# Kernel optimization log

Measured on AMD Instinct MI355X. Metric: run time of the kernel, lower is better.

Reference implementation:

```python
import jax, jax.numpy as jnp
from jax import lax
import numpy as np

WSTD = 0.1
BSTD = 0.1
DN = ("NHWC", "HWIO", "NHWC")  # matches tf.nn.convolution defaults


def setup_inputs() -> dict:
    key = jax.random.key(0)
    k1, k2, k3, k4, k5 = jax.random.split(key, 5)
    B, H, Wd, Cin, F, KH, KW = 32, 64, 64, 128, 256, 3, 3
    X = jax.random.normal(k1, (B, H, Wd, Cin), dtype=jnp.float32)
    # glorot-ish kernel
    fan = KH * KW * Cin
    W = jax.random.normal(k2, (KH, KW, Cin, F), dtype=jnp.float32) / np.float32(np.sqrt(fan))
    bias = 0.01 * jax.random.normal(k3, (F,), dtype=jnp.float32)
    # per-sample multiplicative errors: abs(1 + N(0, std)) as in A-Connect
    Werr = jnp.abs(1.0 + WSTD * jax.random.normal(k4, (B, KH, KW, Cin, F), dtype=jnp.float32))
    Berr = jnp.abs(1.0 + BSTD * jax.random.normal(k5, (B, F), dtype=jnp.float32))
    return {"X": X, "W": W, "bias": bias, "Werr": Werr, "Berr": Berr}


def reference(X, W, bias, Werr, Berr):
    # memW[b] = W * Werr[b]  -> per-sample perturbed kernels [B,KH,KW,Cin,F]
    memW = W[None] * Werr

    def conv1(x, k):  # x: [H,W,Cin], k: [KH,KW,Cin,F]
        return lax.conv_general_dilated(x[None], k, window_strides=(1, 1),
                                        padding="SAME", dimension_numbers=DN)[0]

    Z = jax.vmap(conv1)(X, memW)                 # [B,H,W,F]
    membias = bias[None] * Berr                  # [B,F]
    Z = Z + membias[:, None, None, :]
    return jax.nn.relu(Z)
```

## Files before the change

kernel.cpp:

```cpp
#include <hip/hip_runtime.h>

#define B_   32
#define H_   64
#define W_   64
#define CIN  128
#define F_   256
#define K_   1152
#define M_   4096

#define HP_   66
#define XPROW (66*128)
#define XPIMG (66*66*128)
#define XP_ELEMS ((size_t)B_ * XPIMG)
#define XP_BYTES (XP_ELEMS * 2)

#define WBT_BYTES ((size_t)B_ * F_ * K_ * 2)
#define FULL_WS   (WBT_BYTES + XP_BYTES + 256)
#define ZPAGE_OFF WBT_BYTES

#define BM_ 256
#define BK_ 64

typedef __attribute__((ext_vector_type(8))) short bf16x8;
typedef __attribute__((ext_vector_type(4))) float f32x4;

__device__ __forceinline__ unsigned pkbf(float a, float b) {
    unsigned ua = __builtin_bit_cast(unsigned, a) + 0x8000u;
    unsigned ub = __builtin_bit_cast(unsigned, b) + 0x8000u;
    return __builtin_amdgcn_perm(ub, ua, 0x07060302u);
}

__device__ __forceinline__ void async16(const void* g, void* l) {
    __builtin_amdgcn_global_load_lds(
        (const __attribute__((address_space(1))) unsigned int*)g,
        (__attribute__((address_space(3))) unsigned int*)l, 16, 0, 0);
}

__global__ void prep_kernel(const float* __restrict__ W,
                            const float* __restrict__ Werr,
                            const float* __restrict__ X,
                            unsigned short* __restrict__ WbT,
                            unsigned short* __restrict__ Xp,
                            unsigned int* __restrict__ zpage) {
    __shared__ float tile[32 * 68];
    int bid = blockIdx.x;
    int t   = threadIdx.x;

    if (bid < 4608) {
        int ft   = bid & 3;
        int rest = bid >> 2;
        int kt   = rest % 36;
        int b    = rest / 36;
        int k0 = kt * 32;
        int f0 = ft * 64;

        if (bid == 0 && t < 64) zpage[t] = 0u;

        #pragma unroll
        for (int i = 0; i < 2; ++i) {
            int c   = i * 256 + t;
            int kl  = c >> 4;
            int fl4 = c & 15;
            size_t src = (size_t)(k0 + kl) * F_ + f0 + fl4 * 4;
            f32x4 w4 = *(const f32x4*)&W[src];
            f32x4 e4 = *(const f32x4*)&Werr[(size_t)b * (K_ * F_) + src];
            f32x4 v  = w4 * e4;
            *(f32x4*)&tile[kl * 68 + fl4 * 4] = v;
        }
        __syncthreads();
        {
            int c  = t;
            int fl = c >> 2;
            int ku = c & 3;
            unsigned pk[4];
            #pragma unroll
            for (int j2 = 0; j2 < 4; ++j2) {
                float x0 = tile[(ku * 8 + j2 * 2 + 0) * 68 + fl];
                float x1 = tile[(ku * 8 + j2 * 2 + 1) * 68 + fl];
                pk[j2] = pkbf(x0, x1);
            }
            size_t dst = ((size_t)(b * F_ + f0 + fl)) * K_ + k0 + ku * 8;
            *(uint4*)&WbT[dst] = make_uint4(pk[0], pk[1], pk[2], pk[3]);
        }
    } else {
        int e = (bid - 4608) * 256 + t;
        int c16  = e & 15;
        int pos  = e >> 4;
        int wp   = pos % 66;
        int rest = pos / 66;
        int hp   = rest % 66;
        int b    = rest / 66;
        uint4 out;
        if (hp >= 1 && hp <= 64 && wp >= 1 && wp <= 64) {
            const float* src = X + (((size_t)b * 64 + (hp - 1)) * 64 + (wp - 1)) * 128
                                 + c16 * 8;
            f32x4 a = *(const f32x4*)src;
            f32x4 c = *(const f32x4*)(src + 4);
            out.x = pkbf(a[0], a[1]);  out.y = pkbf(a[2], a[3]);
            out.z = pkbf(c[0], c[1]);  out.w = pkbf(c[2], c[3]);
        } else {
            out = make_uint4(0u, 0u, 0u, 0u);
        }
        *(uint4*)&Xp[(size_t)e * 8] = out;
    }
}

__global__ void wbt_kernel(const float* __restrict__ W,
                           const float* __restrict__ Werr,
                           unsigned short* __restrict__ WbT,
                           unsigned int* __restrict__ zpage) {
    __shared__ float tile[32 * 68];
    int bid = blockIdx.x;
    int ft   = bid & 3;
    int rest = bid >> 2;
    int kt   = rest % 36;
    int b    = rest / 36;
    int k0 = kt * 32;
    int f0 = ft * 64;
    int t  = threadIdx.x;

    if (bid == 0 && t < 64) zpage[t] = 0u;

    #pragma unroll
    for (int i = 0; i < 2; ++i) {
        int c   = i * 256 + t;
        int kl  = c >> 4;
        int fl4 = c & 15;
        size_t src = (size_t)(k0 + kl) * F_ + f0 + fl4 * 4;
        f32x4 w4 = *(const f32x4*)&W[src];
        f32x4 e4 = *(const f32x4*)&Werr[(size_t)b * (K_ * F_) + src];
        f32x4 v  = w4 * e4;
        *(f32x4*)&tile[kl * 68 + fl4 * 4] = v;
    }
    __syncthreads();
    {
        int c  = t;
        int fl = c >> 2;
        int ku = c & 3;
        unsigned pk[4];
        #pragma unroll
        for (int j2 = 0; j2 < 4; ++j2) {
            float x0 = tile[(ku * 8 + j2 * 2 + 0) * 68 + fl];
            float x1 = tile[(ku * 8 + j2 * 2 + 1) * 68 + fl];
            pk[j2] = pkbf(x0, x1);
        }
        size_t dst = ((size_t)(b * F_ + f0 + fl)) * K_ + k0 + ku * 8;
        *(uint4*)&WbT[dst] = make_uint4(pk[0], pk[1], pk[2], pk[3]);
    }
}

__global__ __launch_bounds__(512, 2)
void gemm256_kernel(const unsigned short* __restrict__ Xp,
                    const unsigned short* __restrict__ WbT,
                    const float* __restrict__ bias,
                    const float* __restrict__ Berr,
                    float* __restrict__ Out) {
    __shared__ unsigned short As[2][BM_ * BK_];
    __shared__ unsigned short Bs[2][BM_ * BK_];

    int bid = blockIdx.x;
    int g   = (bid & 7) * 64 + (bid >> 3);
    int b   = g >> 4;
    int mt  = g & 15;
    int pm0 = mt * 256;

    int t    = threadIdx.x;
    int lane = t & 63;
    int wv   = t >> 6;
    int wm   = wv >> 2;
    int wn   = wv & 3;
    int l16  = lane & 15;
    int quad = lane >> 4;
    int swz  = (l16 & 7) << 4;

    const unsigned short* XpB = Xp + (size_t)b * XPIMG;
    const unsigned short* WbB = WbT + (size_t)b * F_ * K_;

    int tr   = t >> 3;
    int sc   = (t & 7) ^ (tr & 7);
    int aoff = tr * 128 + sc * 8;
    int boff = tr * K_ + sc * 8;
    int mbase = mt * 4;
    int ldof = t * 8;

    f32x4 acc[8][4];
    #pragma unroll
    for (int mi = 0; mi < 8; ++mi)
        #pragma unroll
        for (int ni = 0; ni < 4; ++ni)
            acc[mi][ni] = (f32x4){0.f, 0.f, 0.f, 0.f};

    auto stageA = [&](int bs, int ru, int ko) {
        async16(XpB + (size_t)(mbase + ru) * XPROW + aoff + ko,
                &As[bs][ru * 4096 + ldof]);
    };
    auto stageB = [&](int bs, int ru, int ko) {
        async16(WbB + (size_t)ru * (64 * K_) + boff + ko,
                &Bs[bs][ru * 4096 + ldof]);
    };

    stageB(0, 0, 0); stageB(0, 1, 0); stageB(0, 2, 0); stageB(0, 3, 0);
    stageA(0, 0, 0); stageA(0, 2, 0); stageA(0, 1, 0); stageA(0, 3, 0);
    asm volatile("s_waitcnt vmcnt(2)" ::: "memory");
    __builtin_amdgcn_s_barrier();

    for (int kt = 0; kt < 18; ++kt) {
        const int cur = kt & 1;
        const int nxt = cur ^ 1;
        const unsigned short* Ac = As[cur];
        const unsigned short* Bc = Bs[cur];
        const bool pf = (kt < 17);

        int ktn  = kt + 1;
        int khwN = ktn >> 1;
        int khN  = (khwN * 11) >> 5;
        int kwN  = khwN - khN * 3;
        int koA  = khN * XPROW + kwN * 128 + (ktn & 1) * 64;
        int koB  = ktn * 64;

        bf16x8 af[4], bfr[4];

        #pragma unroll
        for (int ni = 0; ni < 4; ++ni) {
            int row = wn * 64 + ni * 16 + l16;
            bfr[ni] = *(const bf16x8*)((const char*)Bc + ((row * 128 + quad * 16) ^ swz));
        }
        #pragma unroll
        for (int mi = 0; mi < 4; ++mi) {
            int row = wm * 128 + mi * 16 + l16;
            af[mi] = *(const bf16x8*)((const char*)Ac + ((row * 128 + quad * 16) ^ swz));
        }
        if (pf) { stageB(nxt, 0, koB); stageB(nxt, 1, koB); }
        __builtin_amdgcn_s_barrier();
        __builtin_amdgcn_s_setprio(1);
        #pragma unroll
        for (int mi = 0; mi < 4; ++mi)
            #pragma unroll
            for (int ni = 0; ni < 4; ++ni)
                acc[mi][ni] = __builtin_amdgcn_mfma_f32_16x16x32_bf16(
                    af[mi], bfr[ni], acc[mi][ni], 0, 0, 0);
        __builtin_amdgcn_s_setprio(0);
        if (pf) asm volatile("s_waitcnt vmcnt(2)" ::: "memory");
        else    asm volatile("s_waitcnt vmcnt(0)" ::: "memory");
        __builtin_amdgcn_s_barrier();

        #pragma unroll
        for (int mi = 0; mi < 4; ++mi) {
            int row = wm * 128 + 64 + mi * 16 + l16;
            af[mi] = *(const bf16x8*)((const char*)Ac + ((row * 128 + quad * 16) ^ swz));
        }
        if (pf) { stageB(nxt, 2, koB); stageB(nxt, 3, koB); }
        __builtin_amdgcn_s_barrier();
        __builtin_amdgcn_s_setprio(1);
        #pragma unroll
        for (int mi = 0; mi < 4; ++mi)
            #pragma unroll
            for (int ni = 0; ni < 4; ++ni)
                acc[4 + mi][ni] = __builtin_amdgcn_mfma_f32_16x16x32_bf16(
                    af[mi], bfr[ni], acc[4 + mi][ni], 0, 0, 0);
        __builtin_amdgcn_s_setprio(0);
        __builtin_amdgcn_s_barrier();

        #pragma unroll
        for (int ni = 0; ni < 4; ++ni) {
            int row = wn * 64 + ni * 16 + l16;
            bfr[ni] = *(const bf16x8*)((const char*)Bc + ((row * 128 + quad * 16 + 64) ^ swz));
        }
        #pragma unroll
        for (int mi = 0; mi < 4; ++mi) {
            int row = wm * 128 + mi * 16 + l16;
            af[mi] = *(const bf16x8*)((const char*)Ac + ((row * 128 + quad * 16 + 64) ^ swz));
        }
        if (pf) { stageA(nxt, 0, koA); stageA(nxt, 2, koA); }
        __builtin_amdgcn_s_barrier();
        __builtin_amdgcn_s_setprio(1);
        #pragma unroll
        for (int mi = 0; mi < 4; ++mi)
            #pragma unroll
            for (int ni = 0; ni < 4; ++ni)
                acc[mi][ni] = __builtin_amdgcn_mfma_f32_16x16x32_bf16(
                    af[mi], bfr[ni], acc[mi][ni], 0, 0, 0);
        __builtin_amdgcn_s_setprio(0);
        __builtin_amdgcn_s_barrier();

        #pragma unroll
        for (int mi = 0; mi < 4; ++mi) {
            int row = wm * 128 + 64 + mi * 16 + l16;
            af[mi] = *(const bf16x8*)((const char*)Ac + ((row * 128 + quad * 16 + 64) ^ swz));
        }
        if (pf) { stageA(nxt, 1, koA); stageA(nxt, 3, koA); }
        __builtin_amdgcn_s_barrier();
        __builtin_amdgcn_s_setprio(1);
        #pragma unroll
        for (int mi = 0; mi < 4; ++mi)
            #pragma unroll
            for (int ni = 0; ni < 4; ++ni)
                acc[4 + mi][ni] = __builtin_amdgcn_mfma_f32_16x16x32_bf16(
                    af[mi], bfr[ni], acc[4 + mi][ni], 0, 0, 0);
        __builtin_amdgcn_s_setprio(0);
        if (pf) asm volatile("s_waitcnt vmcnt(2)" ::: "memory");
        __builtin_amdgcn_s_barrier();
    }

    float mb[4];
    #pragma unroll
    for (int ni = 0; ni < 4; ++ni) {
        int f = wn * 64 + ni * 16 + l16;
        mb[ni] = bias[f] * Berr[b * F_ + f];
    }
    #pragma unroll
    for (int mi = 0; mi < 8; ++mi) {
        #pragma unroll
        for (int rr = 0; rr < 4; ++rr) {
            int mm = pm0 + wm * 128 + mi * 16 + quad * 4 + rr;
            float* orow = Out + ((size_t)b * M_ + mm) * F_ + wn * 64;
            #pragma unroll
            for (int ni = 0; ni < 4; ++ni) {
                float v = acc[mi][ni][rr] + mb[ni];
                orow[ni * 16 + l16] = fmaxf(v, 0.0f);
            }
        }
    }
}

__global__ __launch_bounds__(256, 2)
void gemm_kernel_f32(const float* __restrict__ X,
                     const unsigned short* __restrict__ WbT,
                     const float* __restrict__ zpage,
                     const float* __restrict__ bias,
                     const float* __restrict__ Berr,
                     float* __restrict__ Out) {
    __shared__ unsigned short As[128 * 32];
    __shared__ unsigned short Bs[128 * 32];

    int bid = blockIdx.x;
    int g   = (bid & 7) | ((bid >> 8) << 3);
    int mt  = (bid >> 3) & 31;
    int b   = g >> 1;
    int nt  = g & 1;
    int pm0 = mt * 128;

    int t    = threadIdx.x;
    int lane = t & 63;
    int wv   = t >> 6;
    int wm   = wv >> 1;
    int wn   = wv & 1;
    int l16  = lane & 15;
    int quad = lane >> 4;

    int ml   = t >> 1;
    int half = t & 1;
    int m    = pm0 + ml;
    int hb   = m >> 6;
    int wwv  = m & 63;
    const float* Abase = X + (((size_t)b * 64 + hb - 1) * 64 + (wwv - 1)) * 128
                           + half * 16;
    unsigned vm = 0;
    #pragma unroll
    for (int khw = 0; khw < 9; ++khw) {
        int kh = (khw * 11) >> 5;
        int kw = khw - kh * 3;
        bool ok = ((unsigned)(hb + kh - 1) < 64u) && ((unsigned)(wwv + kw - 1) < 64u);
        vm |= (unsigned)ok << khw;
    }
    int ldsA = ml * 32 + half * 16;

    const unsigned short* wb = WbT + ((size_t)(b * F_ + nt * 128)) * K_;
    const unsigned short* Bbase[2];
    int ldsB[2];
    #pragma unroll
    for (int cc = 0; cc < 2; ++cc) {
        int c   = t + cc * 256;
        int nl  = c >> 2;
        int off = c & 3;
        Bbase[cc] = wb + (size_t)nl * K_ + off * 8;
        ldsB[cc]  = c * 8;
    }

    f32x4 acc[4][4];
    #pragma unroll
    for (int mi = 0; mi < 4; ++mi)
        #pragma unroll
        for (int ni = 0; ni < 4; ++ni)
            acc[mi][ni] = (f32x4){0.f, 0.f, 0.f, 0.f};

    f32x4 pr0, pr1, pr2, pr3;
    {
        const float* p = (vm & 1) ? Abase : zpage;
        pr0 = *(const f32x4*)(p);
        pr1 = *(const f32x4*)(p + 4);
        pr2 = *(const f32x4*)(p + 8);
        pr3 = *(const f32x4*)(p + 12);
    }

    for (int kt = 0; kt < 36; ++kt) {
        uint4 lo, hi;
        lo.x = pkbf(pr0[0], pr0[1]);  lo.y = pkbf(pr0[2], pr0[3]);
        lo.z = pkbf(pr1[0], pr1[1]);  lo.w = pkbf(pr1[2], pr1[3]);
        hi.x = pkbf(pr2[0], pr2[1]);  hi.y = pkbf(pr2[2], pr2[3]);
        hi.z = pkbf(pr3[0], pr3[1]);  hi.w = pkbf(pr3[2], pr3[3]);

        if (kt) __syncthreads();
        *(uint4*)&As[ldsA]     = lo;
        *(uint4*)&As[ldsA + 8] = hi;
        #pragma unroll
        for (int cc = 0; cc < 2; ++cc)
            async16(Bbase[cc] + kt * 32, &Bs[ldsB[cc]]);
        __syncthreads();

        if (kt < 35) {
            int ktn  = kt + 1;
            int khw  = ktn >> 2;
            int kh   = (khw * 11) >> 5;
            int kw   = khw - kh * 3;
            int koff = kh * 8192 + kw * 128 + ((ktn & 3) << 5);
            const float* p = ((vm >> khw) & 1) ? Abase + koff : zpage;
            pr0 = *(const f32x4*)(p);
            pr1 = *(const f32x4*)(p + 4);
            pr2 = *(const f32x4*)(p + 8);
            pr3 = *(const f32x4*)(p + 12);
        }

        bf16x8 af[4], bf[4];
        #pragma unroll
        for (int i = 0; i < 4; ++i) {
            af[i] = *(const bf16x8*)&As[(wm * 64 + i * 16 + l16) * 32 + quad * 8];
            bf[i] = *(const bf16x8*)&Bs[(wn * 64 + i * 16 + l16) * 32 + quad * 8];
        }
        #pragma unroll
        for (int mi = 0; mi < 4; ++mi)
            #pragma unroll
            for (int ni = 0; ni < 4; ++ni)
                acc[mi][ni] = __builtin_amdgcn_mfma_f32_16x16x32_bf16(
                    af[mi], bf[ni], acc[mi][ni], 0, 0, 0);
    }

    float mb[4];
    #pragma unroll
    for (int ni = 0; ni < 4; ++ni) {
        int f = nt * 128 + wn * 64 + ni * 16 + l16;
        mb[ni] = bias[f] * Berr[b * F_ + f];
    }
    #pragma unroll
    for (int mi = 0; mi < 4; ++mi) {
        #pragma unroll
        for (int rr = 0; rr < 4; ++rr) {
            int mm = pm0 + wm * 64 + mi * 16 + quad * 4 + rr;
            float* orow = Out + ((size_t)b * M_ + mm) * F_ + nt * 128 + wn * 64;
            #pragma unroll
            for (int ni = 0; ni < 4; ++ni) {
                float v = acc[mi][ni][rr] + mb[ni];
                orow[ni * 16 + l16] = fmaxf(v, 0.0f);
            }
        }
    }
}

__global__ __launch_bounds__(256)
void fallback_kernel(const float* __restrict__ X, const float* __restrict__ W,
                     const float* __restrict__ bias, const float* __restrict__ Werr,
                     const float* __restrict__ Berr, float* __restrict__ Out) {
    __shared__ float Xs[3 * 66 * 128];
    int bid = blockIdx.x;
    int b = bid >> 6;
    int h = bid & 63;
    int t = threadIdx.x;
    int f = t;

    for (int e = t; e < 3 * 66 * 128; e += 256) {
        int kh  = e / (66 * 128);
        int rem = e - kh * 66 * 128;
        int w66 = rem >> 7;
        int c   = rem & 127;
        int hh = h + kh - 1, ww = w66 - 1;
        float v = 0.f;
        if (hh >= 0 && hh < 64 && ww >= 0 && ww < 64)
            v = X[(((size_t)b * 64 + hh) * 64 + ww) * 128 + c];
        Xs[e] = v;
    }
    __syncthreads();

    float acc[64];
    #pragma unroll
    for (int w = 0; w < 64; ++w) acc[w] = 0.f;

    for (int kk = 0; kk < 9; ++kk) {
        int kh = (kk * 11) >> 5;
        int kw = kk - kh * 3;
        for (int c = 0; c < 128; ++c) {
            size_t wi = ((size_t)kk * 128 + c) * 256 + f;
            float wvv = W[wi] * Werr[(size_t)b * (K_ * F_) + wi];
            const float* xr = &Xs[(kh * 66 + kw) * 128 + c];
            #pragma unroll
            for (int w = 0; w < 64; ++w)
                acc[w] = fmaf(xr[w * 128], wvv, acc[w]);
        }
    }
    float mb = bias[f] * Berr[b * 256 + f];
    for (int w = 0; w < 64; ++w)
        Out[(((size_t)b * 64 + h) * 64 + w) * 256 + f] = fmaxf(acc[w] + mb, 0.f);
}

extern "C" void kernel_launch(void* const* d_in, const int* in_sizes, int n_in,
                              void* d_out, int out_size, void* d_ws, size_t ws_size,
                              hipStream_t stream) {
    const float* X    = (const float*)d_in[0];
    const float* W    = (const float*)d_in[1];
    const float* bias = (const float*)d_in[2];
    const float* Werr = (const float*)d_in[3];
    const float* Berr = (const float*)d_in[4];
    float* Out = (float*)d_out;

    if (ws_size >= FULL_WS) {
        unsigned short* WbT = (unsigned short*)d_ws;
        unsigned short* Xp  = (unsigned short*)((char*)d_ws + WBT_BYTES);
        unsigned int*   zpg = (unsigned int*)((char*)d_ws + WBT_BYTES + XP_BYTES);
        prep_kernel<<<4608 + 8712, 256, 0, stream>>>(W, Werr, X, WbT, Xp, zpg);
        gemm256_kernel<<<512, 512, 0, stream>>>(Xp, WbT, bias, Berr, Out);
    } else if (ws_size >= WBT_BYTES + 256) {
        unsigned short* WbT  = (unsigned short*)d_ws;
        unsigned int*   zpg  = (unsigned int*)((char*)d_ws + ZPAGE_OFF);
        wbt_kernel<<<B_ * 36 * 4, 256, 0, stream>>>(W, Werr, WbT, zpg);
        gemm_kernel_f32<<<B_ * 32 * 2, 256, 0, stream>>>(X, WbT, (const float*)zpg,
                                                         bias, Berr, Out);
    } else {
        fallback_kernel<<<B_ * 64, 256, 0, stream>>>(X, W, bias, Werr, Berr, Out);
    }
}
```

Baseline: 297.0 us.

## Restructure GEMM k-loop: fewer barriers, batched async staging, separate fragment registers

The inner k-tile loop drops from eight workgroup barriers per iteration to two. Each half of the tile's async global-to-LDS copies for B and A is now issued in one batch instead of being spread across four phases. Distinct register fragments (a0..a3, b0, b1) are kept so LDS reads can be grouped and MFMAs issued back-to-back, and sched_barrier pins the compiler ordering. This cuts barrier stalls at the cost of higher VGPR pressure and less interleaving of copies with compute.

Result: faster. 289.3 us (-2.6%).

```diff
diff --git a/kernel.cpp b/kernel.cpp
--- a/kernel.cpp
+++ b/kernel.cpp
@@ -203,6 +203,7 @@
     stageA(0, 0, 0); stageA(0, 2, 0); stageA(0, 1, 0); stageA(0, 3, 0);
     asm volatile("s_waitcnt vmcnt(2)" ::: "memory");
     __builtin_amdgcn_s_barrier();
+    __builtin_amdgcn_sched_barrier(0);
 
     for (int kt = 0; kt < 18; ++kt) {
         const int cur = kt & 1;
@@ -218,88 +219,90 @@
         int koA  = khN * XPROW + kwN * 128 + (ktn & 1) * 64;
         int koB  = ktn * 64;
 
-        bf16x8 af[4], bfr[4];
-
+        bf16x8 b0[4], a0[4];
         #pragma unroll
         for (int ni = 0; ni < 4; ++ni) {
             int row = wn * 64 + ni * 16 + l16;
-            bfr[ni] = *(const bf16x8*)((const char*)Bc + ((row * 128 + quad * 16) ^ swz));
+            b0[ni] = *(const bf16x8*)((const char*)Bc + ((row * 128 + quad * 16) ^ swz));
         }
         #pragma unroll
         for (int mi = 0; mi < 4; ++mi) {
             int row = wm * 128 + mi * 16 + l16;
-            af[mi] = *(const bf16x8*)((const char*)Ac + ((row * 128 + quad * 16) ^ swz));
-        }
-        if (pf) { stageB(nxt, 0, koB); stageB(nxt, 1, koB); }
-        __builtin_amdgcn_s_barrier();
+            a0[mi] = *(const bf16x8*)((const char*)Ac + ((row * 128 + quad * 16) ^ swz));
+        }
+        if (pf) {
+            stageB(nxt, 0, koB); stageB(nxt, 1, koB);
+            stageB(nxt, 2, koB); stageB(nxt, 3, koB);
+        }
         __builtin_amdgcn_s_setprio(1);
         #pragma unroll
         for (int mi = 0; mi < 4; ++mi)
             #pragma unroll
             for (int ni = 0; ni < 4; ++ni)
                 acc[mi][ni] = __builtin_amdgcn_mfma_f32_16x16x32_bf16(
-                    af[mi], bfr[ni], acc[mi][ni], 0, 0, 0);
+                    a0[mi], b0[ni], acc[mi][ni], 0, 0, 0);
         __builtin_amdgcn_s_setprio(0);
-        if (pf) asm volatile("s_waitcnt vmcnt(2)" ::: "memory");
+
+        if (pf) asm volatile("s_waitcnt vmcnt(4)" ::: "memory");
         else    asm volatile("s_waitcnt vmcnt(0)" ::: "memory");
         __builtin_amdgcn_s_barrier();
-
+        __builtin_amdgcn_sched_barrier(0);
+
+        bf16x8 a1[4];
         #pragma unroll
         for (int mi = 0; mi < 4; ++mi) {
             int row = wm * 128 + 64 + mi * 16 + l16;
-            af[mi] = *(const bf16x8*)((const char*)Ac + ((row * 128 + quad * 16) ^ swz));
-        }
-        if (pf) { stageB(nxt, 2, koB); stageB(nxt, 3, koB); }
-        __builtin_amdgcn_s_barrier();
+            a1[mi] = *(const bf16x8*)((const char*)Ac + ((row * 128 + quad * 16) ^ swz));
+        }
+        if (pf) {
+            stageA(nxt, 0, koA); stageA(nxt, 2, koA);
+            stageA(nxt, 1, koA); stageA(nxt, 3, koA);
+        }
         __builtin_amdgcn_s_setprio(1);
         #pragma unroll
         for (int mi = 0; mi < 4; ++mi)
             #pragma unroll
             for (int ni = 0; ni < 4; ++ni)
                 acc[4 + mi][ni] = __builtin_amdgcn_mfma_f32_16x16x32_bf16(
-                    af[mi], bfr[ni], acc[4 + mi][ni], 0, 0, 0);
+                    a1[mi], b0[ni], acc[4 + mi][ni], 0, 0, 0);
         __builtin_amdgcn_s_setprio(0);
-        __builtin_amdgcn_s_barrier();
-
+
+        bf16x8 b1[4], a2[4], a3[4];
         #pragma unroll
         for (int ni = 0; ni < 4; ++ni) {
             int row = wn * 64 + ni * 16 + l16;
-            bfr[ni] = *(const bf16x8*)((const char*)Bc + ((row * 128 + quad * 16 + 64) ^ swz));
+            b1[ni] = *(const bf16x8*)((const char*)Bc + ((row * 128 + quad * 16 + 64) ^ swz));
         }
         #pragma unroll
         for (int mi = 0; mi < 4; ++mi) {
             int row = wm * 128 + mi * 16 + l16;
-            af[mi] = *(const bf16x8*)((const char*)Ac + ((row * 128 + quad * 16 + 64) ^ swz));
-        }
-        if (pf) { stageA(nxt, 0, koA); stageA(nxt, 2, koA); }
-        __builtin_amdgcn_s_barrier();
+            a2[mi] = *(const bf16x8*)((const char*)Ac + ((row * 128 + quad * 16 + 64) ^ swz));
+        }
+        #pragma unroll
+        for (int mi = 0; mi < 4; ++mi) {
+            int row = wm * 128 + 64 + mi * 16 + l16;
+            a3[mi] = *(const bf16x8*)((const char*)Ac + ((row * 128 + quad * 16 + 64) ^ swz));
+        }
         __builtin_amdgcn_s_setprio(1);
         #pragma unroll
         for (int mi = 0; mi < 4; ++mi)
             #pragma unroll
             for (int ni = 0; ni < 4; ++ni)
                 acc[mi][ni] = __builtin_amdgcn_mfma_f32_16x16x32_bf16(
-                    af[mi], bfr[ni], acc[mi][ni], 0, 0, 0);
-        __builtin_amdgcn_s_setprio(0);
-        __builtin_amdgcn_s_barrier();
-
-        #pragma unroll
-        for (int mi = 0; mi < 4; ++mi) {
-            int row = wm * 128 + 64 + mi * 16 + l16;
-            af[mi] = *(const bf16x8*)((const char*)Ac + ((row * 128 + quad * 16 + 64) ^ swz));
-        }
-        if (pf) { stageA(nxt, 1, koA); stageA(nxt, 3, koA); }
-        __builtin_amdgcn_s_barrier();
-        __builtin_amdgcn_s_setprio(1);
+                    a2[mi], b1[ni], acc[mi][ni], 0, 0, 0);
         #pragma unroll
         for (int mi = 0; mi < 4; ++mi)
             #pragma unroll
             for (int ni = 0; ni < 4; ++ni)
                 acc[4 + mi][ni] = __builtin_amdgcn_mfma_f32_16x16x32_bf16(
-                    af[mi], bfr[ni], acc[4 + mi][ni], 0, 0, 0);
+                    a3[mi], b1[ni], acc[4 + mi][ni], 0, 0, 0);
         __builtin_amdgcn_s_setprio(0);
-        if (pf) asm volatile("s_waitcnt vmcnt(2)" ::: "memory");
-        __builtin_amdgcn_s_barrier();
+
+        if (pf) {
+            asm volatile("s_waitcnt vmcnt(2)" ::: "memory");
+            __builtin_amdgcn_s_barrier();
+            __builtin_amdgcn_sched_barrier(0);
+        }
     }
 
     float mb[4];
```
